# Performance work log

Measured on AMD Instinct MI355X. Metric: run time of the kernel, lower is better.

The kernel has to match this reference:

```python
import jax, jax.numpy as jnp
import numpy as np

B, T = 8, 1024
IN_FEAT = 1024
N_FEAT = 1024
N_HEAD = 16
D_K = N_FEAT // N_HEAD
KERNEL = 11
LEFT_PAD = (KERNEL - 1) // 2  # sanm_shift=0
RIGHT_PAD = KERNEL - 1 - LEFT_PAD


def setup_inputs() -> dict:
    key = jax.random.key(0)
    ks = jax.random.split(key, 7)
    hidden_states = jax.random.normal(ks[0], (B, T, IN_FEAT), dtype=jnp.float32)
    mask = jax.random.randint(ks[1], (B, 1, T), 0, 2, dtype=jnp.int32)
    s_qkv = 1.0 / np.sqrt(IN_FEAT)
    s_out = 1.0 / np.sqrt(N_FEAT)
    W_qkv = jax.random.normal(ks[2], (3 * N_FEAT, IN_FEAT), dtype=jnp.float32) * s_qkv
    b_qkv = jnp.zeros((3 * N_FEAT,), dtype=jnp.float32)
    W_out = jax.random.normal(ks[3], (N_FEAT, N_FEAT), dtype=jnp.float32) * s_out
    b_out = jnp.zeros((N_FEAT,), dtype=jnp.float32)
    fsmn_kernel = jax.random.normal(ks[4], (N_FEAT, 1, KERNEL), dtype=jnp.float32) * (1.0 / KERNEL)
    return {"hidden_states": hidden_states, "mask": mask, "W_qkv": W_qkv,
            "b_qkv": b_qkv, "W_out": W_out, "b_out": b_out, "fsmn_kernel": fsmn_kernel}


def _fsmn(v, maskf, fsmn_kernel):
    # v: [B,T,D], maskf: [B,T,1]
    vm = v * maskf
    x = jnp.transpose(vm, (0, 2, 1))  # [B,D,T]
    x = jnp.pad(x, ((0, 0), (0, 0), (LEFT_PAD, RIGHT_PAD)))
    # depthwise conv1d (cross-correlation, matching torch Conv1d)
    y = jax.lax.conv_general_dilated(
        x, fsmn_kernel, window_strides=(1,), padding='VALID',
        dimension_numbers=('NCH', 'OIH', 'NCH'), feature_group_count=N_FEAT)
    y = jnp.transpose(y, (0, 2, 1)) + vm  # [B,T,D]
    return y * maskf


def reference(hidden_states, mask, W_qkv, b_qkv, W_out, b_out, fsmn_kernel):
    b, t, _ = hidden_states.shape
    qkv = jnp.einsum('btf,of->bto', hidden_states, W_qkv) + b_qkv  # [B,T,3*N_FEAT]
    q, k, v = jnp.split(qkv, 3, axis=-1)
    def heads(x):
        return jnp.transpose(x.reshape(b, t, N_HEAD, D_K), (0, 2, 1, 3))  # [B,H,T,D_K]
    q_h, k_h, v_h = heads(q), heads(k), heads(v)

    maskf = mask.reshape(b, t, 1).astype(hidden_states.dtype)
    fsmn_memory = _fsmn(v, maskf, fsmn_kernel)

    scale = D_K ** -0.5
    scores = jnp.einsum('bhqd,bhkd->bhqk', q_h * scale, k_h)  # [B,H,T,T]
    mask_keys = (mask.reshape(b, 1, 1, t) == 0)  # True where padded
    scores = jnp.where(mask_keys, -jnp.inf, scores)
    attn = jax.nn.softmax(scores, axis=-1)
    attn = jnp.where(mask_keys, 0.0, attn)
    ctx = jnp.einsum('bhqk,bhkd->bhqd', attn, v_h)  # [B,H,T,D_K]
    ctx = jnp.transpose(ctx, (0, 2, 1, 3)).reshape(b, t, N_FEAT)
    att_outs = jnp.einsum('btf,of->bto', ctx, W_out) + b_out
    return att_outs + fsmn_memory
```

## Files before the change

kernel.cpp:

```cpp
#include <hip/hip_runtime.h>
#include <stdint.h>


typedef uint16_t u16;
typedef float f32x4 __attribute__((ext_vector_type(4)));
typedef __bf16 bf16x8 __attribute__((ext_vector_type(8)));
typedef __bf16 bf16x2 __attribute__((ext_vector_type(2)));
typedef u16 u16x8 __attribute__((ext_vector_type(8)));
typedef u16 u16x4 __attribute__((ext_vector_type(4)));
typedef short s16x4 __attribute__((ext_vector_type(4)));

__device__ __forceinline__ u16 f2bf(float f) {
    union { float f; uint32_t u; } c; c.f = f;
    uint32_t u = c.u;
    return (u16)((u + 0x7fffu + ((u >> 16) & 1u)) >> 16);
}
__device__ __forceinline__ float bf2f(u16 h) {
    union { uint32_t u; float f; } c; c.u = ((uint32_t)h) << 16;
    return c.f;
}
__device__ __forceinline__ uint32_t pack_bf16(float a, float b) {
    bf16x2 t; t[0] = (__bf16)a; t[1] = (__bf16)b;
    union { bf16x2 v; uint32_t u; } c; c.v = t; return c.u;
}

__global__ __launch_bounds__(256) void cvt_all(const float* __restrict__ hs,
                                               const float* __restrict__ wqkv,
                                               const float* __restrict__ wout,
                                               u16* __restrict__ hsb,
                                               u16* __restrict__ wqkvb,
                                               u16* __restrict__ woutb) {
    int bid = blockIdx.x;
    const float* src; u16* dst; int ib;
    if (bid < 8192)       { src = hs;   dst = hsb;   ib = bid; }
    else if (bid < 11264) { src = wqkv; dst = wqkvb; ib = bid - 8192; }
    else                  { src = wout; dst = woutb; ib = bid - 11264; }
    int i = (ib * 256 + threadIdx.x) * 4;
    float4 v = *reinterpret_cast<const float4*>(src + i);
    ushort4 o;
    o.x = f2bf(v.x); o.y = f2bf(v.y); o.z = f2bf(v.z); o.w = f2bf(v.w);
    *reinterpret_cast<ushort4*>(dst + i) = o;
}

__global__ void mask_and_kt(const int* __restrict__ mask, uint32_t* __restrict__ mb,
                            const float* __restrict__ fk, float* __restrict__ kt) {
    int bid = blockIdx.x;
    if (bid < 44) {
        int idx = bid * 256 + threadIdx.x;
        int j = idx >> 10, c = idx & 1023;
        kt[idx] = fk[c * 11 + j];
    } else {
        int i = threadIdx.x;
        int b = i >> 5, c = i & 31;
        uint32_t u = 0;
        for (int j = 0; j < 32; ++j)
            u |= (mask[(b << 10) + c * 32 + j] ? 1u : 0u) << j;
        mb[i] = u;
    }
}

template<int MODE>
__global__ __launch_bounds__(512, 4) void gemm_bk32(
    const u16* __restrict__ A, const u16* __restrict__ Bw, int M, int N, int K,
    int ntiles_n, const float* __restrict__ bias,
    u16* __restrict__ qo, u16* __restrict__ ko, u16* __restrict__ vo,
    float* __restrict__ out)
{
    __shared__ u16 lds[36864];
    const int t = threadIdx.x;
    const int lane = t & 63;
    const int wave = t >> 6;
    const int wr = wave >> 2, wc = wave & 3;
    const int lr = lane & 15, lq = lane >> 4;
    const int r3 = lane >> 2, c4 = lane & 3;
    const int cpx = gridDim.x >> 3;
    const int bid = (blockIdx.x & 7) * cpx + (blockIdx.x >> 3);
    const int m0 = (bid / ntiles_n) * 128;
    const int n0 = (bid % ntiles_n) * 256;
    const int NT = K >> 5;

    const u16* AgW  = A  + (size_t)(m0 + wave * 16 + r3) * K + c4 * 8;
    const u16* BgW0 = Bw + (size_t)(n0 + wave * 16 + r3) * K + c4 * 8;
    const u16* BgW1 = BgW0 + (size_t)128 * K;

    auto stage = [&](int buf, int tile) {
        u16* dA  = lds + buf * 12288 + wave * 512;
        u16* dB0 = lds + buf * 12288 + 4096 + wave * 512;
        u16* dB1 = dB0 + 4096;
        __builtin_amdgcn_global_load_lds(
            (const __attribute__((address_space(1))) void*)(AgW + tile * 32),
            (__attribute__((address_space(3))) void*)dA, 16, 0, 0);
        __builtin_amdgcn_global_load_lds(
            (const __attribute__((address_space(1))) void*)(BgW0 + tile * 32),
            (__attribute__((address_space(3))) void*)dB0, 16, 0, 0);
        __builtin_amdgcn_global_load_lds(
            (const __attribute__((address_space(1))) void*)(BgW1 + tile * 32),
            (__attribute__((address_space(3))) void*)dB1, 16, 0, 0);
    };

    f32x4 acc[4][4];
#pragma unroll
    for (int i = 0; i < 4; ++i)
#pragma unroll
        for (int j = 0; j < 4; ++j) acc[i][j] = (f32x4){0.f, 0.f, 0.f, 0.f};

    stage(0, 0);
    stage(1, 1);
    asm volatile("s_waitcnt vmcnt(3)" ::: "memory");
    __builtin_amdgcn_s_barrier();

    for (int T = 0; T < NT; ++T) {
        const int bcur = T % 3;
        const u16* Ab = lds + bcur * 12288;
        const u16* Bb = Ab + 4096;
        bf16x8 a[4], bb[4];
#pragma unroll
        for (int mm = 0; mm < 4; ++mm)
            a[mm] = *reinterpret_cast<const bf16x8*>(Ab + (wr * 64 + mm * 16 + lr) * 32 + lq * 8);
#pragma unroll
        for (int nn = 0; nn < 4; ++nn)
            bb[nn] = *reinterpret_cast<const bf16x8*>(Bb + (wc * 64 + nn * 16 + lr) * 32 + lq * 8);
        if (T + 2 < NT) stage((T + 2) % 3, T + 2);
        __builtin_amdgcn_s_setprio(1);
#pragma unroll
        for (int mm = 0; mm < 4; ++mm)
#pragma unroll
            for (int nn = 0; nn < 4; ++nn)
                acc[mm][nn] = __builtin_amdgcn_mfma_f32_16x16x32_bf16(a[mm], bb[nn], acc[mm][nn], 0, 0, 0);
        __builtin_amdgcn_s_setprio(0);
        if (T + 2 < NT)      asm volatile("s_waitcnt vmcnt(3)" ::: "memory");
        else if (T + 1 < NT) asm volatile("s_waitcnt vmcnt(0)" ::: "memory");
        if (T + 1 < NT) __builtin_amdgcn_s_barrier();
    }

    if (MODE == 0 && n0 >= 2048) {
        __syncthreads();
        u16* patch = lds + wave * 4608;
#pragma unroll
        for (int m = 0; m < 4; ++m)
#pragma unroll
            for (int n = 0; n < 4; ++n) {
                int c = n * 16 + lr;
                int rrl = m * 16 + lq * 4;
#pragma unroll
                for (int r = 0; r < 4; ++r)
                    patch[c * 72 + rrl + r] = f2bf(acc[m][n][r]);
            }
        const int col0 = n0 + wc * 64;
        const int row0 = m0 + wr * 64;
#pragma unroll
        for (int p = 0; p < 8; ++p) {
            int c = p * 8 + (lane >> 3);
            int tch = (lane & 7) * 8;
            u16x8 v = *reinterpret_cast<const u16x8*>(patch + c * 72 + tch);
            int col = col0 + c;
            int cc = col & 1023;
            int h = cc >> 6, d = cc & 63;
            int rg = row0 + tch;
            int b = rg >> 10, tt = rg & 1023;
            *reinterpret_cast<u16x8*>(vo + (((size_t)(b * 16 + h)) << 16) +
                                      (size_t)d * 1024 + tt) = v;
        }
    } else {
#pragma unroll
        for (int m = 0; m < 4; ++m) {
            int row = m0 + wr * 64 + m * 16 + lq * 4;
#pragma unroll
            for (int n = 0; n < 4; ++n) {
                int col = n0 + wc * 64 + n * 16 + lr;
                float bv = bias[col];
#pragma unroll
                for (int r = 0; r < 4; ++r) {
                    float val = acc[m][n][r] + bv;
                    int rr = row + r;
                    if (MODE == 0) {
                        int part = col >> 10;
                        int cc = col & 1023;
                        int h = cc >> 6, d = cc & 63;
                        int b = rr >> 10, tt = rr & 1023;
                        size_t bh = (size_t)(b * 16 + h);
                        u16* dst = (part == 0) ? qo : ko;
                        dst[((bh << 10) + tt) * 64 + d] = f2bf(part == 0 ? val * 0.18033688011f : val);
                    } else {
                        size_t o = (size_t)rr * N + col;
                        out[o] = val + bf2f(vo[o]);
                    }
                }
            }
        }
    }
}

__global__ __launch_bounds__(256) void fsmn_v4(const u16* __restrict__ vt,
                                               const int* __restrict__ mask,
                                               const float* __restrict__ kt,
                                               u16* __restrict__ fsb)
{
    __shared__ float vs[64][147];
    __shared__ float ms[144];
    const int tid = threadIdx.x;
    const int tc = blockIdx.x & 7;
    const int bh = blockIdx.x >> 3;
    const int b = bh >> 4, h = bh & 15;
    const int t0 = tc * 128;
    const u16* vrow = vt + ((size_t)bh << 16);
    const int* mrow = mask + (b << 10);

    if (tid < 144) {
        int tt = t0 - 8 + tid;
        ms[tid] = (tt >= 0 && tt < 1024) ? (float)mrow[tt] : 0.f;
    }
    const int sd = tid >> 2;
    const int ci0 = tid & 3;
#pragma unroll
    for (int it = 0; it < 5; ++it) {
        int ci = ci0 + it * 4;
        if (ci < 18) {
            int tbase = t0 - 8 + ci * 8;
            if (tbase >= 0 && tbase < 1024) {
                u16x8 v8 = *reinterpret_cast<const u16x8*>(vrow + (size_t)sd * 1024 + tbase);
#pragma unroll
                for (int j = 0; j < 8; ++j)
                    vs[sd][ci * 8 + j] = bf2f((u16)v8[j]) * (float)mrow[tbase + j];
            } else {
#pragma unroll
                for (int j = 0; j < 8; ++j) vs[sd][ci * 8 + j] = 0.f;
            }
        }
    }
    __syncthreads();

    const int dd = tid & 63;
    const int tg = tid >> 6;
    const int c = h * 64 + dd;
    float kc[11];
#pragma unroll
    for (int j = 0; j < 11; ++j) kc[j] = kt[j * 1024 + c];

    const int tl0 = tg * 32;
    float w[11];
#pragma unroll
    for (int j = 0; j < 11; ++j) w[j] = vs[dd][3 + tl0 + j];
    u16* orow = fsb + ((size_t)(b * 1024 + t0 + tl0)) * 1024 + c;
#pragma unroll 4
    for (int s = 0; s < 32; ++s) {
        float acc = 0.f;
#pragma unroll
        for (int j = 0; j < 11; ++j) acc += kc[j] * w[j];
        float mf = ms[8 + tl0 + s];
        orow[(size_t)s * 1024] = f2bf((acc + w[5]) * mf);
#pragma unroll
        for (int j = 0; j < 10; ++j) w[j] = w[j + 1];
        w[10] = vs[dd][3 + tl0 + s + 11];
    }
}

__global__ __launch_bounds__(256) void attn_v11(const u16* __restrict__ qg,
                                                const u16* __restrict__ kg,
                                                const u16* __restrict__ vtg,
                                                const uint32_t* __restrict__ mbits,
                                                u16* __restrict__ ctx)
{
    __shared__ u16 K_s[2][64 * 64];
    __shared__ u16 V_s[2][64 * 64];
    const int t = threadIdx.x;
    const int lane = t & 63;
    const int w = t >> 6;
    const int lr = lane & 15, lq = lane >> 4;
    const int bh = blockIdx.x & 127;
    const int qc = blockIdx.x >> 7;
    const int b = bh >> 4, h = bh & 15;
    const size_t base = (size_t)bh << 16;
    const u16* kb = kg + base;
    const u16* vb = vtg + base;
    const int q0 = qc * 128 + w * 32;

    bf16x8 qf[2][2];
#pragma unroll
    for (int qt = 0; qt < 2; ++qt)
#pragma unroll
        for (int kk = 0; kk < 2; ++kk)
            qf[qt][kk] = *reinterpret_cast<const bf16x8*>(
                qg + base + (size_t)(q0 + qt * 16 + lr) * 64 + kk * 32 + lq * 8);

    f32x4 oacc[2][4];
    f32x4 oacc_l[2];
#pragma unroll
    for (int qt = 0; qt < 2; ++qt) {
        oacc_l[qt] = (f32x4){0.f, 0.f, 0.f, 0.f};
#pragma unroll
        for (int dt = 0; dt < 4; ++dt) oacc[qt][dt] = (f32x4){0.f, 0.f, 0.f, 0.f};
    }

    s16x4 ones_f;
#pragma unroll
    for (int j = 0; j < 4; ++j) ones_f[j] = (short)0x3F80;

    const uint32_t* mrow = mbits + b * 32;

    auto stage = [&](int bufi, int tile) {
        const int k0s = tile * 64;
#pragma unroll
        for (int rd = 0; rd < 2; ++rd) {
            int ch = rd * 256 + w * 64 + lane;
            int row = ch >> 3, c7 = ch & 7;
            int sc = (c7 ^ (row & 7)) * 8;
            const u16* srcK = kb + (size_t)(k0s + row) * 64 + sc;
            const u16* srcV = vb + (size_t)row * 1024 + k0s + sc;
            u16* dK = &K_s[bufi][(size_t)(rd * 256 + w * 64) * 8];
            u16* dV = &V_s[bufi][(size_t)(rd * 256 + w * 64) * 8];
            __builtin_amdgcn_global_load_lds(
                (const __attribute__((address_space(1))) void*)srcK,
                (__attribute__((address_space(3))) void*)dK, 16, 0, 0);
            __builtin_amdgcn_global_load_lds(
                (const __attribute__((address_space(1))) void*)srcV,
                (__attribute__((address_space(3))) void*)dV, 16, 0, 0);
        }
    };

    stage(0, 0);
    asm volatile("s_waitcnt vmcnt(0)");
    __syncthreads();

    for (int it = 0; it < 16; ++it) {
        const u16* Kb = K_s[it & 1];
        const u16* Vb = V_s[it & 1];
        if (it < 15) stage((it + 1) & 1, it + 1);

        bf16x8 kf[4][2];
#pragma unroll
        for (int kt = 0; kt < 4; ++kt) {
            int row = kt * 16 + lr;
#pragma unroll
            for (int kk = 0; kk < 2; ++kk) {
                int g = (kk * 4 + lq) ^ (row & 7);
                kf[kt][kk] = *reinterpret_cast<const bf16x8*>(Kb + row * 64 + g * 8);
            }
        }

        const uint32_t mw0 = mrow[it * 2], mw1 = mrow[it * 2 + 1];
        uint32_t mb_[4];
        mb_[0] = mw0 >> (lq * 4);
        mb_[1] = mw0 >> (16 + lq * 4);
        mb_[2] = mw1 >> (lq * 4);
        mb_[3] = mw1 >> (16 + lq * 4);
        f32x4 ma[4];
#pragma unroll
        for (int kt = 0; kt < 4; ++kt)
#pragma unroll
            for (int r = 0; r < 4; ++r)
                ma[kt][r] = (mb_[kt] & (1u << r)) ? 0.f : -3e38f;

        s16x4 vf[4][4];
#pragma unroll
        for (int ks = 0; ks < 4; ++ks)
#pragma unroll
            for (int dt = 0; dt < 4; ++dt) {
                int row = dt * 16 + lr;
                int g = (ks * 2 + (lq >> 1)) ^ (row & 7);
                vf[ks][dt] = *reinterpret_cast<const s16x4*>(Vb + row * 64 + g * 8 + (lq & 1) * 4);
            }

#pragma unroll
        for (int qt = 0; qt < 2; ++qt) {
            f32x4 s[4];
            __builtin_amdgcn_s_setprio(1);
#pragma unroll
            for (int kt = 0; kt < 4; ++kt) {
                s[kt] = __builtin_amdgcn_mfma_f32_16x16x32_bf16(kf[kt][0], qf[qt][0], ma[kt], 0, 0, 0);
                s[kt] = __builtin_amdgcn_mfma_f32_16x16x32_bf16(kf[kt][1], qf[qt][1], s[kt], 0, 0, 0);
            }
            __builtin_amdgcn_s_setprio(0);

            union { uint32_t u[2]; s16x4 v; } pa[4];
#pragma unroll
            for (int kt = 0; kt < 4; ++kt) {
                float p0 = __builtin_amdgcn_exp2f(s[kt][0]);
                float p1 = __builtin_amdgcn_exp2f(s[kt][1]);
                float p2 = __builtin_amdgcn_exp2f(s[kt][2]);
                float p3 = __builtin_amdgcn_exp2f(s[kt][3]);
                pa[kt].u[0] = pack_bf16(p0, p1);
                pa[kt].u[1] = pack_bf16(p2, p3);
            }

            __builtin_amdgcn_s_setprio(1);
#pragma unroll
            for (int dt = 0; dt < 4; ++dt) {
                f32x4 o = oacc[qt][dt];
#pragma unroll
                for (int kt = 0; kt < 4; ++kt)
                    o = __builtin_amdgcn_mfma_f32_16x16x16bf16_1k(vf[kt][dt], pa[kt].v, o, 0, 0, 0);
                oacc[qt][dt] = o;
            }
#pragma unroll
            for (int kt = 0; kt < 4; ++kt)
                oacc_l[qt] = __builtin_amdgcn_mfma_f32_16x16x16bf16_1k(ones_f, pa[kt].v, oacc_l[qt], 0, 0, 0);
            __builtin_amdgcn_s_setprio(0);
        }

        if (it < 15) {
            asm volatile("s_waitcnt vmcnt(0)" ::: "memory");
            __syncthreads();
        }
    }

#pragma unroll
    for (int qt = 0; qt < 2; ++qt) {
        float li = 1.f / oacc_l[qt][0];
        int trow = q0 + qt * 16 + lr;
        u16* crow = ctx + ((size_t)(b << 10) + trow) * 1024 + h * 64;
#pragma unroll
        for (int dt = 0; dt < 4; ++dt) {
            f32x4 o = oacc[qt][dt];
            u16x4 pkv;
            pkv[0] = f2bf(o[0] * li); pkv[1] = f2bf(o[1] * li);
            pkv[2] = f2bf(o[2] * li); pkv[3] = f2bf(o[3] * li);
            *reinterpret_cast<u16x4*>(crow + dt * 16 + lq * 4) = pkv;
        }
    }
}

extern "C" void kernel_launch(void* const* d_in, const int* in_sizes, int n_in,
                              void* d_out, int out_size, void* d_ws, size_t ws_size,
                              hipStream_t stream)
{
    (void)in_sizes; (void)n_in; (void)out_size; (void)ws_size;
    const float* hs   = (const float*)d_in[0];
    const int*   mask = (const int*)d_in[1];
    const float* Wqkv = (const float*)d_in[2];
    const float* bqkv = (const float*)d_in[3];
    const float* Wout = (const float*)d_in[4];
    const float* bout = (const float*)d_in[5];
    const float* fk   = (const float*)d_in[6];
    float* out = (float*)d_out;

    char* ws = (char*)d_ws;
    u16* hsb   = (u16*)(ws);
    u16* wqkvb = (u16*)(ws + 16777216);
    u16* woutb = (u16*)(ws + 23068672);
    u16* qb    = (u16*)(ws + 25165824);
    u16* kb    = (u16*)(ws + 41943040);
    u16* vtb   = (u16*)(ws + 58720256);
    u16* ctxb  = (u16*)(ws + 75497472);
    uint32_t* mbits = (uint32_t*)ws;
    float* ktT = (float*)(ws + 4096);
    u16* fsb   = (u16*)(ws + 65536);

    cvt_all<<<12288, 256, 0, stream>>>(hs, Wqkv, Wout, hsb, wqkvb, woutb);

    gemm_bk32<0><<<64 * 12, 512, 0, stream>>>(hsb, wqkvb, 8192, 3072, 1024, 12,
                                              bqkv, qb, kb, vtb, nullptr);
    mask_and_kt<<<45, 256, 0, stream>>>(mask, mbits, fk, ktT);
    fsmn_v4<<<1024, 256, 0, stream>>>(vtb, mask, ktT, fsb);
    attn_v11<<<1024, 256, 0, stream>>>(qb, kb, vtb, mbits, ctxb);
    gemm_bk32<1><<<64 * 4, 512, 0, stream>>>(ctxb, woutb, 8192, 1024, 1024, 4,
                                             bout, nullptr, nullptr, fsb, out);
}
```

Before: 178.2 us.

## Replace output projection GEMM with 128x128-tile triple-buffered kernel

```diff
diff --git a/kernel.cpp b/kernel.cpp
--- a/kernel.cpp
+++ b/kernel.cpp
@@ -173,19 +173,103 @@
                 for (int r = 0; r < 4; ++r) {
                     float val = acc[m][n][r] + bv;
                     int rr = row + r;
-                    if (MODE == 0) {
-                        int part = col >> 10;
-                        int cc = col & 1023;
-                        int h = cc >> 6, d = cc & 63;
-                        int b = rr >> 10, tt = rr & 1023;
-                        size_t bh = (size_t)(b * 16 + h);
-                        u16* dst = (part == 0) ? qo : ko;
-                        dst[((bh << 10) + tt) * 64 + d] = f2bf(part == 0 ? val * 0.18033688011f : val);
-                    } else {
-                        size_t o = (size_t)rr * N + col;
-                        out[o] = val + bf2f(vo[o]);
-                    }
+                    int part = col >> 10;
+                    int cc = col & 1023;
+                    int h = cc >> 6, d = cc & 63;
+                    int b = rr >> 10, tt = rr & 1023;
+                    size_t bh = (size_t)(b * 16 + h);
+                    u16* dst = (part == 0) ? qo : ko;
+                    dst[((bh << 10) + tt) * 64 + d] = f2bf(part == 0 ? val * 0.18033688011f : val);
                 }
+            }
+        }
+    }
+}
+
+__global__ __launch_bounds__(256, 4) void gemm_sq128(
+    const u16* __restrict__ A, const u16* __restrict__ Bw, int M, int N, int K,
+    int ntiles_n, const float* __restrict__ bias,
+    const u16* __restrict__ fsb, float* __restrict__ out)
+{
+    __shared__ u16 lds[24576];
+    const int t = threadIdx.x;
+    const int lane = t & 63;
+    const int wave = t >> 6;
+    const int wr = wave >> 1, wc = wave & 1;
+    const int lr = lane & 15, lq = lane >> 4;
+    const int r3 = lane >> 2, c4 = lane & 3;
+    const int cpx = gridDim.x >> 3;
+    const int bid = (blockIdx.x & 7) * cpx + (blockIdx.x >> 3);
+    const int m0 = (bid / ntiles_n) * 128;
+    const int n0 = (bid % ntiles_n) * 128;
+    const int NT = K >> 5;
+
+    const u16* AgW = A  + (size_t)(m0 + wave * 16 + r3) * K + c4 * 8;
+    const u16* BgW = Bw + (size_t)(n0 + wave * 16 + r3) * K + c4 * 8;
+
+    auto stage = [&](int buf, int tile) {
+        u16* dA = lds + buf * 8192 + wave * 512;
+        u16* dB = lds + buf * 8192 + 4096 + wave * 512;
+        __builtin_amdgcn_global_load_lds(
+            (const __attribute__((address_space(1))) void*)(AgW + tile * 32),
+            (__attribute__((address_space(3))) void*)dA, 16, 0, 0);
+        __builtin_amdgcn_global_load_lds(
+            (const __attribute__((address_space(1))) void*)(AgW + (size_t)64 * K + tile * 32),
+            (__attribute__((address_space(3))) void*)(dA + 2048), 16, 0, 0);
+        __builtin_amdgcn_global_load_lds(
+            (const __attribute__((address_space(1))) void*)(BgW + tile * 32),
+            (__attribute__((address_space(3))) void*)dB, 16, 0, 0);
+        __builtin_amdgcn_global_load_lds(
+            (const __attribute__((address_space(1))) void*)(BgW + (size_t)64 * K + tile * 32),
+            (__attribute__((address_space(3))) void*)(dB + 2048), 16, 0, 0);
+    };
+
+    f32x4 acc[4][4];
+#pragma unroll
+    for (int i = 0; i < 4; ++i)
+#pragma unroll
+        for (int j = 0; j < 4; ++j) acc[i][j] = (f32x4){0.f, 0.f, 0.f, 0.f};
+
+    stage(0, 0);
+    stage(1, 1);
+    asm volatile("s_waitcnt vmcnt(4)" ::: "memory");
+    __builtin_amdgcn_s_barrier();
+
+    for (int T = 0; T < NT; ++T) {
+        const int bcur = T % 3;
+        const u16* Ab = lds + bcur * 8192;
+        const u16* Bb = Ab + 4096;
+        bf16x8 a[4], bb[4];
+#pragma unroll
+        for (int mm = 0; mm < 4; ++mm)
+            a[mm] = *reinterpret_cast<const bf16x8*>(Ab + (wr * 64 + mm * 16 + lr) * 32 + lq * 8);
+#pragma unroll
+        for (int nn = 0; nn < 4; ++nn)
+            bb[nn] = *reinterpret_cast<const bf16x8*>(Bb + (wc * 64 + nn * 16 + lr) * 32 + lq * 8);
+        if (T + 2 < NT) stage((T + 2) % 3, T + 2);
+        __builtin_amdgcn_s_setprio(1);
+#pragma unroll
+        for (int mm = 0; mm < 4; ++mm)
+#pragma unroll
+            for (int nn = 0; nn < 4; ++nn)
+                acc[mm][nn] = __builtin_amdgcn_mfma_f32_16x16x32_bf16(a[mm], bb[nn], acc[mm][nn], 0, 0, 0);
+        __builtin_amdgcn_s_setprio(0);
+        if (T + 2 < NT)      asm volatile("s_waitcnt vmcnt(4)" ::: "memory");
+        else if (T + 1 < NT) asm volatile("s_waitcnt vmcnt(0)" ::: "memory");
+        if (T + 1 < NT) __builtin_amdgcn_s_barrier();
+    }
+
+#pragma unroll
+    for (int m = 0; m < 4; ++m) {
+        int row = m0 + wr * 64 + m * 16 + lq * 4;
+#pragma unroll
+        for (int n = 0; n < 4; ++n) {
+            int col = n0 + wc * 64 + n * 16 + lr;
+            float bv = bias[col];
+#pragma unroll
+            for (int r = 0; r < 4; ++r) {
+                size_t o = (size_t)(row + r) * N + col;
+                out[o] = acc[m][n][r] + bv + bf2f(fsb[o]);
             }
         }
     }
@@ -453,6 +537,6 @@
     mask_and_kt<<<45, 256, 0, stream>>>(mask, mbits, fk, ktT);
     fsmn_v4<<<1024, 256, 0, stream>>>(vtb, mask, ktT, fsb);
     attn_v11<<<1024, 256, 0, stream>>>(qb, kb, vtb, mbits, ctxb);
-    gemm_bk32<1><<<64 * 4, 512, 0, stream>>>(ctxb, woutb, 8192, 1024, 1024, 4,
-                                             bout, nullptr, nullptr, fsb, out);
-}
+    gemm_sq128<<<64 * 8, 256, 0, stream>>>(ctxb, woutb, 8192, 1024, 1024, 8,
+                                           bout, fsb, out);
+}
```

New measurement: 178.0 us. About the same (-0.1%).
